# Kernel optimization log

Measured on AMD Instinct MI355X. Metric: run time of the kernel, lower is better.

## Reference

```python
import jax, jax.numpy as jnp
import numpy as np

B, S, D, E, H, K = 4, 2048, 1024, 8, 512, 2


def setup_inputs() -> dict:
    key = jax.random.key(0)
    ks = jax.random.split(key, 11)
    sc = 0.02
    return {
        "x": jax.random.normal(ks[0], (B, S, D), dtype=jnp.float32),
        "gate_W": jax.random.normal(ks[1], (D, E), dtype=jnp.float32) * sc,
        "W1": jax.random.normal(ks[2], (E, D, H), dtype=jnp.float32) * sc,
        "b1": jnp.zeros((E, H), dtype=jnp.float32),
        "W2": jax.random.normal(ks[3], (E, H, D), dtype=jnp.float32) * sc,
        "b2": jnp.zeros((E, D), dtype=jnp.float32),
        "Ws1": jax.random.normal(ks[4], (D, H), dtype=jnp.float32) * sc,
        "bs1": jnp.zeros((H,), dtype=jnp.float32),
        "Ws2": jax.random.normal(ks[5], (H, D), dtype=jnp.float32) * sc,
        "bs2": jnp.zeros((D,), dtype=jnp.float32),
        "route_scale": jnp.ones((), dtype=jnp.float32),
    }


def reference(x, gate_W, W1, b1, W2, b2, Ws1, bs1, Ws2, bs2, route_scale):
    # Gating: sigmoid scores scaled by route_scale (score_func='sigmoid')
    scores = jax.nn.sigmoid(x @ gate_W) * route_scale          # (B,S,E)
    topk_scores, topk_idx = jax.lax.top_k(scores, K)           # (B,S,K)
    topk_w = topk_scores / topk_scores.sum(-1, keepdims=True)  # normalized weights
    # Dense combine weights: zero for non-selected experts (same math as
    # the original sparse gather/scatter loop).
    onehot = jax.nn.one_hot(topk_idx, E, dtype=x.dtype)        # (B,S,K,E)
    gate_full = jnp.einsum('bsk,bske->bse', topk_w, onehot)    # (B,S,E)
    # Per-expert MLP applied to all tokens, combined with sparse gate weights.
    h = jax.nn.gelu(jnp.einsum('bsd,edh->bseh', x, W1) + b1, approximate=False)
    y = jnp.einsum('bseh,ehd->bsed', h, W2) + b2               # (B,S,E,D)
    expert_out = jnp.einsum('bse,bsed->bsd', gate_full, y)     # (B,S,D)
    # Shared expert MLP (always active)
    shared = jax.nn.gelu(x @ Ws1 + bs1, approximate=False) @ Ws2 + bs2
    return expert_out + shared
```

## Files before the change

kernel.cpp:

```cpp
#include <hip/hip_runtime.h>
#include <hip/hip_bf16.h>

#define TOKENS 8192
#define D_DIM  1024
#define E_NUM  8
#define H_DIM  512
#define N1     4608
#define CAP    3072
#define ET256  (CAP / 256)
#define EXP_ROWS (E_NUM * CAP)
#define SH_BASE  EXP_ROWS
#define HS_ROWS (EXP_ROWS + TOKENS)

typedef __bf16 bf16_t;
typedef __bf16 bf16x8 __attribute__((ext_vector_type(8)));
typedef __bf16 bf16x4 __attribute__((ext_vector_type(4)));
typedef float  f32x4  __attribute__((ext_vector_type(4)));

__device__ __forceinline__ float gelu_fast(float v) {
  float w = v * v;
  float t = __builtin_fmaf(w, 0.10294307f, 2.30258835f);
  float z = v * t;
  float e = __builtin_amdgcn_exp2f(z);
  float r = __builtin_amdgcn_rcpf(e + 1.0f);
  return v - v * r;
}

__global__ __launch_bounds__(256) void routing_repack_kernel(
    const float* __restrict__ x, const float* __restrict__ gW,
    const float* __restrict__ route_scale, float* __restrict__ gateT,
    int* __restrict__ sel, bf16_t* __restrict__ Xb,
    const float* __restrict__ W1, const float* __restrict__ Ws1,
    const float* __restrict__ W2, const float* __restrict__ Ws2,
    bf16_t* __restrict__ Bt1, bf16_t* __restrict__ Bt2e) {
  const int bid = blockIdx.x;
  if (bid < TOKENS / 4) {
    int tok  = bid * 4 + (threadIdx.x >> 6);
    int lane = threadIdx.x & 63;
    const float* xr = x + (size_t)tok * D_DIM;
    double p[E_NUM];
#pragma unroll
    for (int e = 0; e < E_NUM; ++e) p[e] = 0.0;
    for (int d = lane; d < D_DIM; d += 64) {
      double xv = (double)xr[d];
      const float* g = gW + (size_t)d * E_NUM;
#pragma unroll
      for (int e = 0; e < E_NUM; ++e) p[e] += xv * (double)g[e];
    }
#pragma unroll
    for (int off = 32; off > 0; off >>= 1) {
#pragma unroll
      for (int e = 0; e < E_NUM; ++e) p[e] += __shfl_xor(p[e], off, 64);
    }
    if (lane == 0) {
      double rs = (double)route_scale[0];
      double s[E_NUM];
#pragma unroll
      for (int e = 0; e < E_NUM; ++e) s[e] = rs / (1.0 + exp(-p[e]));
      int i1 = 0;
#pragma unroll
      for (int e = 1; e < E_NUM; ++e) if (s[e] > s[i1]) i1 = e;
      int i2 = (i1 == 0) ? 1 : 0;
#pragma unroll
      for (int e = 0; e < E_NUM; ++e) if (e != i1 && s[e] > s[i2]) i2 = e;
      double inv = 1.0 / (s[i1] + s[i2]);
      float o[E_NUM];
#pragma unroll
      for (int e = 0; e < E_NUM; ++e) o[e] = 0.f;
      o[i1] = (float)(s[i1] * inv);
      o[i2] = (float)(s[i2] * inv);
#pragma unroll
      for (int e = 0; e < E_NUM; ++e) gateT[(size_t)e * TOKENS + tok] = o[e];
      sel[tok] = i1 * 8 + i2;
    }
    const float4* x4 = (const float4*)xr;
    bf16x4* xb4 = (bf16x4*)(Xb + (size_t)tok * D_DIM);
#pragma unroll
    for (int i = 0; i < 4; ++i) {
      float4 v = x4[i * 64 + lane];
      bf16x4 o = { (bf16_t)v.x, (bf16_t)v.y, (bf16_t)v.z, (bf16_t)v.w };
      xb4[i * 64 + lane] = o;
    }
  } else {
    __shared__ float tile[32][33];
    const int rid = bid - TOKENS / 4;
    const int bx = rid & 31, by = rid >> 5;
    const int tx = threadIdx.x & 31, ty = threadIdx.x >> 5;
    if (by < 144) {
      const int k0 = bx * 32, n0 = by * 32;
#pragma unroll
      for (int i = 0; i < 4; ++i) {
        int kl = ty + i * 8;
        int n = n0 + tx, k = k0 + kl;
        float v;
        if (n0 < 4096) v = W1[(size_t)(n >> 9) * (D_DIM * H_DIM) + (size_t)k * H_DIM + (n & 511)];
        else           v = Ws1[(size_t)k * H_DIM + (n - 4096)];
        tile[kl][tx] = v;
      }
      __syncthreads();
#pragma unroll
      for (int i = 0; i < 4; ++i) {
        int nl = ty + i * 8;
        Bt1[(size_t)(n0 + nl) * D_DIM + k0 + tx] = (bf16_t)tile[tx][nl];
      }
    } else {
      const int yy = by - 144;
      const int e = yy >> 4;
      const int h0 = (yy & 15) * 32;
      const int d0 = bx * 32;
#pragma unroll
      for (int i = 0; i < 4; ++i) {
        int hl = ty + i * 8;
        int h = h0 + hl, d = d0 + tx;
        float v = (e < E_NUM) ? W2[((size_t)e * H_DIM + h) * D_DIM + d]
                              : Ws2[(size_t)h * D_DIM + d];
        tile[hl][tx] = v;
      }
      __syncthreads();
#pragma unroll
      for (int i = 0; i < 4; ++i) {
        int dl = ty + i * 8;
        Bt2e[((size_t)e * D_DIM + (d0 + dl)) * H_DIM + h0 + tx] = (bf16_t)tile[tx][dl];
      }
    }
  }
}

__global__ __launch_bounds__(256) void listbuild_kernel(
    const float* __restrict__ gateT, const int* __restrict__ sel,
    int* __restrict__ perm, float* __restrict__ grow,
    int* __restrict__ tok2row, int* __restrict__ padcnt) {
  const int e = blockIdx.x;
  const int tid = threadIdx.x, lane = tid & 63, wid = tid >> 6;
  __shared__ int wsum[4];
  const float* row = gateT + (size_t)e * TOKENS;
  const int base = e * CAP;
  int running = 0;
  float gv = row[tid];
  for (int c = 0; c < TOKENS / 256; ++c) {
    float gv_next = (c + 1 < TOKENS / 256) ? row[(c + 1) * 256 + tid] : 0.f;
    const int tok = c * 256 + tid;
    const bool f = gv > 0.f;
    unsigned long long m = __ballot(f);
    int lanepre = __popcll(m & ((1ull << lane) - 1ull));
    if (lane == 0) wsum[wid] = __popcll(m);
    __syncthreads();
    int wbase = 0;
#pragma unroll
    for (int w2 = 0; w2 < 4; ++w2) if (w2 < wid) wbase += wsum[w2];
    const int tot = wsum[0] + wsum[1] + wsum[2] + wsum[3];
    if (f) {
      const int idx = running + wbase + lanepre;
      if (idx < CAP) {
        perm[base + idx] = tok;
        grow[base + idx] = gv;
        const int s = sel[tok];
        const int other = ((s >> 3) == e) ? (s & 7) : (s >> 3);
        tok2row[tok * 2 + (e > other ? 1 : 0)] = base + idx;
      }
    }
    running += tot;
    __syncthreads();
    gv = gv_next;
  }
  if (running > CAP) running = CAP;
  const int pc = (running + 255) & ~255;
  for (int i = running + tid; i < pc; i += 256) { perm[base + i] = 0; grow[base + i] = 0.f; }
  if (tid == 0) padcnt[e] = pc;
}

__device__ __forceinline__ void gload16(const char* src, char* dst) {
  __builtin_amdgcn_global_load_lds((const __attribute__((address_space(1))) void*)src,
      (__attribute__((address_space(3))) void*)dst, 16, 0, 0);
}

__device__ __forceinline__ void gemm_core256(
    const char* ga0, const char* ga1, const char* ga2, const char* ga3,
    const char* gb0, const char* gb1, const char* gb2, const char* gb3,
    int ktiles, char* lds, int wid, int lane, f32x4 (&acc)[8][4]) {
  const int wm = wid >> 2, wn = wid & 3;
  const int lA = lane & 15, kq = lane >> 4;
  const int slot0 = (kq ^ (lA & 7)) * 16;
  const int slot1 = ((4 + kq) ^ (lA & 7)) * 16;

  auto stage8 = [&](int buf, int t) {
    char* dA = lds + buf * 65536 + wid * 1024;
    char* dB = dA + 32768;
    const size_t ko = (size_t)t * 128;
    gload16(ga0 + ko, dA + 0 * 8192);
    gload16(ga1 + ko, dA + 1 * 8192);
    gload16(ga2 + ko, dA + 2 * 8192);
    gload16(ga3 + ko, dA + 3 * 8192);
    gload16(gb0 + ko, dB + 0 * 8192);
    gload16(gb1 + ko, dB + 1 * 8192);
    gload16(gb2 + ko, dB + 2 * 8192);
    gload16(gb3 + ko, dB + 3 * 8192);
  };

  stage8(0, 0);
  for (int t = 0; t < ktiles; ++t) {
    const int b = t & 1;
    asm volatile("s_waitcnt vmcnt(0)" ::: "memory");
    __builtin_amdgcn_s_barrier();
    asm volatile("" ::: "memory");
    if (t + 1 < ktiles) stage8(b ^ 1, t + 1);
    const char* Ab = lds + b * 65536 + wm * 16384;
    const char* Bb = lds + b * 65536 + 32768 + (wn >> 1) * 16384 + ((wn & 1) * 64) * 128;
    bf16x8 bfv[4][2], af[8][2];
#pragma unroll
    for (int nf = 0; nf < 4; ++nf) {
      const int rb = (nf * 16 + lA) * 128;
      bfv[nf][0] = *(const bf16x8*)(Bb + rb + slot0);
      bfv[nf][1] = *(const bf16x8*)(Bb + rb + slot1);
    }
#pragma unroll
    for (int i = 0; i < 8; ++i) {
      const int ra = (i * 16 + lA) * 128;
      af[i][0] = *(const bf16x8*)(Ab + ra + slot0);
      af[i][1] = *(const bf16x8*)(Ab + ra + slot1);
    }
    __builtin_amdgcn_s_setprio(1);
#pragma unroll
    for (int s = 0; s < 2; ++s)
#pragma unroll
      for (int i = 0; i < 8; ++i)
#pragma unroll
        for (int nf = 0; nf < 4; ++nf)
          acc[i][nf] = __builtin_amdgcn_mfma_f32_16x16x32_bf16(
              af[i][s], bfv[nf][s], acc[i][nf], 0, 0, 0);
    __builtin_amdgcn_s_setprio(0);
  }
}

__device__ __forceinline__ int swz_src(int lane) {
  return ((lane & 7) ^ ((lane >> 3) & 7)) * 16;
}

__global__ __launch_bounds__(512, 2) void gemm1e_kernel(
    const bf16_t* __restrict__ Xb, const bf16_t* __restrict__ Bt1,
    const int* __restrict__ perm, const float* __restrict__ grow,
    const int* __restrict__ padcnt,
    const float* __restrict__ b1, const float* __restrict__ bs1,
    bf16_t* __restrict__ Hs) {
  __shared__ bf16_t sL[65536];
  const int t = threadIdx.x, wid = t >> 6, lane = t & 63;
  const int L = blockIdx.x + 2 * blockIdx.y;
  const int xc = L & 7, ii = L >> 3;
  const int bx = xc >> 2;
  const int by = (xc & 3) * 32 + ii;
  int e, rowbase;
  if (by < E_NUM * ET256) {
    e = by / ET256;
    const int lt = by - e * ET256;
    if (lt * 256 >= padcnt[e]) return;
    rowbase = e * CAP + lt * 256;
  } else {
    e = E_NUM;
    rowbase = SH_BASE + (by - E_NUM * ET256) * 256;
  }
  const int n0 = bx * 256;
  const int rl = wid * 8 + (lane >> 3);
  const int sc = swz_src(lane);
  const char *ga[4], *gb[4];
#pragma unroll
  for (int g = 0; g < 4; ++g) {
    const int r = g * 64 + rl;
    const int tok = (e < E_NUM) ? perm[rowbase + r] : (rowbase - SH_BASE + r);
    ga[g] = (const char*)Xb + (size_t)tok * 2048 + sc;
    gb[g] = (const char*)(Bt1 + (size_t)e * H_DIM * D_DIM) + (size_t)(n0 + r) * 2048 + sc;
  }
  f32x4 acc[8][4];
#pragma unroll
  for (int i = 0; i < 8; ++i)
#pragma unroll
    for (int j = 0; j < 4; ++j) acc[i][j] = (f32x4){0.f, 0.f, 0.f, 0.f};
  gemm_core256(ga[0], ga[1], ga[2], ga[3], gb[0], gb[1], gb[2], gb[3],
               D_DIM / 64, (char*)sL, wid, lane, acc);

  const int wm = wid >> 2, wn = wid & 3, lA = lane & 15;
  const float* bias = (e < E_NUM) ? (b1 + e * H_DIM) : bs1;
#pragma unroll
  for (int mf = 0; mf < 8; ++mf) {
    const int rloc = wm * 128 + mf * 16 + (lane >> 4) * 4;
    float gr[4];
#pragma unroll
    for (int q = 0; q < 4; ++q)
      gr[q] = (e < E_NUM) ? grow[rowbase + rloc + q] : 1.0f;
#pragma unroll
    for (int nf = 0; nf < 4; ++nf) {
      const int col = n0 + wn * 64 + nf * 16 + lA;
      const float bv = bias[col];
#pragma unroll
      for (int q = 0; q < 4; ++q) {
        float v = gelu_fast(acc[mf][nf][q] + bv);
        Hs[(size_t)(rowbase + rloc + q) * H_DIM + col] = (bf16_t)(v * gr[q]);
      }
    }
  }
}

__global__ __launch_bounds__(512, 2) void gemm2e_kernel(
    const bf16_t* __restrict__ Hs, const bf16_t* __restrict__ Bt2e,
    const float* __restrict__ grow, const int* __restrict__ padcnt,
    const float* __restrict__ b2, bf16_t* __restrict__ Ys) {
  __shared__ bf16_t sL[65536];
  const int t = threadIdx.x, wid = t >> 6, lane = t & 63;
  const int L = blockIdx.x + 4 * blockIdx.y;
  const int xc = L & 7, ii = L >> 3;
  const int bx = xc >> 1;
  const int by = (xc & 1) * 48 + ii;
  const int e = by / ET256;
  const int lt = by - e * ET256;
  if (lt * 256 >= padcnt[e]) return;
  const int rowbase = e * CAP + lt * 256;
  const int n0 = bx * 256;
  const int rl = wid * 8 + (lane >> 3);
  const int sc = swz_src(lane);
  const char *ga[4], *gb[4];
#pragma unroll
  for (int g = 0; g < 4; ++g) {
    const int r = g * 64 + rl;
    ga[g] = (const char*)Hs + (size_t)(rowbase + r) * 1024 + sc;
    gb[g] = (const char*)(Bt2e + (size_t)e * D_DIM * H_DIM) + (size_t)(n0 + r) * 1024 + sc;
  }
  f32x4 acc[8][4];
#pragma unroll
  for (int i = 0; i < 8; ++i)
#pragma unroll
    for (int j = 0; j < 4; ++j) acc[i][j] = (f32x4){0.f, 0.f, 0.f, 0.f};
  gemm_core256(ga[0], ga[1], ga[2], ga[3], gb[0], gb[1], gb[2], gb[3],
               H_DIM / 64, (char*)sL, wid, lane, acc);

  const int wm = wid >> 2, wn = wid & 3, lA = lane & 15;
  const float* bb = b2 + (size_t)e * D_DIM;
#pragma unroll
  for (int mf = 0; mf < 8; ++mf) {
    const int rloc = wm * 128 + mf * 16 + (lane >> 4) * 4;
    float gr[4];
#pragma unroll
    for (int q = 0; q < 4; ++q) gr[q] = grow[rowbase + rloc + q];
#pragma unroll
    for (int nf = 0; nf < 4; ++nf) {
      const int col = n0 + wn * 64 + nf * 16 + lA;
      const float bv = bb[col];
#pragma unroll
      for (int q = 0; q < 4; ++q)
        Ys[(size_t)(rowbase + rloc + q) * D_DIM + col] = (bf16_t)(acc[mf][nf][q] + gr[q] * bv);
    }
  }
}

__global__ __launch_bounds__(512, 2) void gemm2s_kernel(
    const bf16_t* __restrict__ Hs, const bf16_t* __restrict__ Bt2e,
    const int* __restrict__ tok2row, const float* __restrict__ bs2,
    const bf16_t* __restrict__ Ys, float* __restrict__ out) {
  __shared__ bf16_t sL[65536];
  const int t = threadIdx.x, wid = t >> 6, lane = t & 63;
  const int L = blockIdx.x + 4 * blockIdx.y;
  const int xc = L & 7, ii = L >> 3;
  const int bx = xc >> 1;
  const int by = (xc & 1) * 16 + ii;
  const int tokbase = by * 256;
  const int rowbase = SH_BASE + tokbase;
  const int n0 = bx * 256;
  const int rl = wid * 8 + (lane >> 3);
  const int sc = swz_src(lane);
  const char *ga[4], *gb[4];
#pragma unroll
  for (int g = 0; g < 4; ++g) {
    const int r = g * 64 + rl;
    ga[g] = (const char*)Hs + (size_t)(rowbase + r) * 1024 + sc;
    gb[g] = (const char*)(Bt2e + (size_t)E_NUM * D_DIM * H_DIM) + (size_t)(n0 + r) * 1024 + sc;
  }
  f32x4 acc[8][4];
#pragma unroll
  for (int i = 0; i < 8; ++i)
#pragma unroll
    for (int j = 0; j < 4; ++j) acc[i][j] = (f32x4){0.f, 0.f, 0.f, 0.f};
  gemm_core256(ga[0], ga[1], ga[2], ga[3], gb[0], gb[1], gb[2], gb[3],
               H_DIM / 64, (char*)sL, wid, lane, acc);

  const int wm = wid >> 2, wn = wid & 3, lA = lane & 15;
#pragma unroll
  for (int mf = 0; mf < 8; ++mf) {
    const int rloc = wm * 128 + mf * 16 + (lane >> 4) * 4;
    int r0[4], r1[4];
#pragma unroll
    for (int q = 0; q < 4; ++q) {
      const int tok = tokbase + rloc + q;
      r0[q] = tok2row[tok * 2];
      r1[q] = tok2row[tok * 2 + 1];
    }
#pragma unroll
    for (int nf = 0; nf < 4; ++nf) {
      const int col = n0 + wn * 64 + nf * 16 + lA;
      const float bv = bs2[col];
#pragma unroll
      for (int q = 0; q < 4; ++q) {
        const int tok = tokbase + rloc + q;
        float y0 = (float)Ys[(size_t)r0[q] * D_DIM + col];
        float y1 = (float)Ys[(size_t)r1[q] * D_DIM + col];
        out[(size_t)tok * D_DIM + col] = acc[mf][nf][q] + bv + y0 + y1;
      }
    }
  }
}

extern "C" void kernel_launch(void* const* d_in, const int* in_sizes, int n_in,
                              void* d_out, int out_size, void* d_ws, size_t ws_size,
                              hipStream_t stream) {
  (void)in_sizes; (void)n_in; (void)out_size; (void)ws_size;
  const float* x    = (const float*)d_in[0];
  const float* gW   = (const float*)d_in[1];
  const float* W1   = (const float*)d_in[2];
  const float* b1   = (const float*)d_in[3];
  const float* W2   = (const float*)d_in[4];
  const float* b2   = (const float*)d_in[5];
  const float* Ws1  = (const float*)d_in[6];
  const float* bs1  = (const float*)d_in[7];
  const float* Ws2  = (const float*)d_in[8];
  const float* bs2  = (const float*)d_in[9];
  const float* rsc  = (const float*)d_in[10];
  float* out = (float*)d_out;

  char* w = (char*)d_ws;
  float*  gateT = (float*)w;  w += (size_t)E_NUM * TOKENS * 4;
  int*    sel   = (int*)w;    w += (size_t)TOKENS * 4;
  bf16_t* Xb    = (bf16_t*)w; w += (size_t)TOKENS * D_DIM * 2;
  bf16_t* Bt1   = (bf16_t*)w; w += (size_t)N1 * D_DIM * 2;
  bf16_t* Bt2e  = (bf16_t*)w; w += (size_t)9 * D_DIM * H_DIM * 2;
  bf16_t* Hs    = (bf16_t*)w; w += (size_t)HS_ROWS * H_DIM * 2;
  bf16_t* Ys    = (bf16_t*)w; w += (size_t)EXP_ROWS * D_DIM * 2;
  int*    perm  = (int*)w;    w += (size_t)EXP_ROWS * 4;
  float*  grow  = (float*)w;  w += (size_t)EXP_ROWS * 4;
  int*    tok2row = (int*)w;  w += (size_t)TOKENS * 2 * 4;
  int*    padcnt  = (int*)w;

  routing_repack_kernel<<<TOKENS / 4 + 32 * 288, 256, 0, stream>>>(
      x, gW, rsc, gateT, sel, Xb, W1, Ws1, W2, Ws2, Bt1, Bt2e);
  listbuild_kernel<<<E_NUM, 256, 0, stream>>>(gateT, sel, perm, grow, tok2row, padcnt);

  gemm1e_kernel<<<dim3(H_DIM / 256, E_NUM * ET256 + TOKENS / 256), dim3(512), 0, stream>>>(
      Xb, Bt1, perm, grow, padcnt, b1, bs1, Hs);
  gemm2e_kernel<<<dim3(D_DIM / 256, E_NUM * ET256), dim3(512), 0, stream>>>(
      Hs, Bt2e, grow, padcnt, b2, Ys);
  gemm2s_kernel<<<dim3(D_DIM / 256, TOKENS / 256), dim3(512), 0, stream>>>(
      Hs, Bt2e, tok2row, bs2, Ys, out);
}
```

Before: 168.4 us.

## Shrink shared-expert GEMM2 tile to 128 rows and split A-fragment loads

```diff
diff --git a/kernel.cpp b/kernel.cpp
--- a/kernel.cpp
+++ b/kernel.cpp
@@ -206,7 +206,7 @@
     if (t + 1 < ktiles) stage8(b ^ 1, t + 1);
     const char* Ab = lds + b * 65536 + wm * 16384;
     const char* Bb = lds + b * 65536 + 32768 + (wn >> 1) * 16384 + ((wn & 1) * 64) * 128;
-    bf16x8 bfv[4][2], af[8][2];
+    bf16x8 bfv[4][2];
 #pragma unroll
     for (int nf = 0; nf < 4; ++nf) {
       const int rb = (nf * 16 + lA) * 128;
@@ -214,21 +214,87 @@
       bfv[nf][1] = *(const bf16x8*)(Bb + rb + slot1);
     }
 #pragma unroll
-    for (int i = 0; i < 8; ++i) {
-      const int ra = (i * 16 + lA) * 128;
-      af[i][0] = *(const bf16x8*)(Ab + ra + slot0);
-      af[i][1] = *(const bf16x8*)(Ab + ra + slot1);
-    }
-    __builtin_amdgcn_s_setprio(1);
-#pragma unroll
-    for (int s = 0; s < 2; ++s)
-#pragma unroll
-      for (int i = 0; i < 8; ++i)
-#pragma unroll
-        for (int nf = 0; nf < 4; ++nf)
-          acc[i][nf] = __builtin_amdgcn_mfma_f32_16x16x32_bf16(
-              af[i][s], bfv[nf][s], acc[i][nf], 0, 0, 0);
-    __builtin_amdgcn_s_setprio(0);
+    for (int qm = 0; qm < 2; ++qm) {
+      bf16x8 af[4][2];
+#pragma unroll
+      for (int i = 0; i < 4; ++i) {
+        const int ra = ((qm * 4 + i) * 16 + lA) * 128;
+        af[i][0] = *(const bf16x8*)(Ab + ra + slot0);
+        af[i][1] = *(const bf16x8*)(Ab + ra + slot1);
+      }
+      __builtin_amdgcn_s_setprio(1);
+#pragma unroll
+      for (int s = 0; s < 2; ++s)
+#pragma unroll
+        for (int i = 0; i < 4; ++i)
+#pragma unroll
+          for (int nf = 0; nf < 4; ++nf)
+            acc[qm * 4 + i][nf] = __builtin_amdgcn_mfma_f32_16x16x32_bf16(
+                af[i][s], bfv[nf][s], acc[qm * 4 + i][nf], 0, 0, 0);
+      __builtin_amdgcn_s_setprio(0);
+      __builtin_amdgcn_sched_barrier(0);
+    }
+  }
+}
+
+__device__ __forceinline__ void gemm_core_s(
+    const char* ga, const char* gb,
+    int ktiles, char* lds, int wid, int lane, f32x4 (&acc)[4][4]) {
+  const int wm = wid >> 2, wn = wid & 3;
+  const int lA = lane & 15, kq = lane >> 4;
+  const int slot0 = (kq ^ (lA & 7)) * 16;
+  const int slot1 = ((4 + kq) ^ (lA & 7)) * 16;
+
+  auto stage6 = [&](int buf, int t) {
+    char* base = lds + buf * 49152;
+    char* dA = base + wid * 2048;
+    char* dB = base + 16384 + wid * 4096;
+    const size_t ko = (size_t)t * 128;
+    gload16(ga + ko,         dA);
+    gload16(ga + 8192 + ko,  dA + 1024);
+    gload16(gb + ko,         dB);
+    gload16(gb + 8192 + ko,  dB + 1024);
+    gload16(gb + 16384 + ko, dB + 2048);
+    gload16(gb + 24576 + ko, dB + 3072);
+  };
+
+  stage6(0, 0);
+  for (int t = 0; t < ktiles; ++t) {
+    const int b = t & 1;
+    asm volatile("s_waitcnt vmcnt(0)" ::: "memory");
+    __builtin_amdgcn_s_barrier();
+    asm volatile("" ::: "memory");
+    if (t + 1 < ktiles) stage6(b ^ 1, t + 1);
+    const char* Ab = lds + b * 49152 + wm * 8192;
+    const char* Bb = lds + b * 49152 + 16384 + wn * 8192;
+    bf16x8 bfv[4][2];
+#pragma unroll
+    for (int nf = 0; nf < 4; ++nf) {
+      const int rb = (nf * 16 + lA) * 128;
+      bfv[nf][0] = *(const bf16x8*)(Bb + rb + slot0);
+      bfv[nf][1] = *(const bf16x8*)(Bb + rb + slot1);
+    }
+#pragma unroll
+    for (int qm = 0; qm < 2; ++qm) {
+      bf16x8 af[2][2];
+#pragma unroll
+      for (int i = 0; i < 2; ++i) {
+        const int ra = ((qm * 2 + i) * 16 + lA) * 128;
+        af[i][0] = *(const bf16x8*)(Ab + ra + slot0);
+        af[i][1] = *(const bf16x8*)(Ab + ra + slot1);
+      }
+      __builtin_amdgcn_s_setprio(1);
+#pragma unroll
+      for (int s = 0; s < 2; ++s)
+#pragma unroll
+        for (int i = 0; i < 2; ++i)
+#pragma unroll
+          for (int nf = 0; nf < 4; ++nf)
+            acc[qm * 2 + i][nf] = __builtin_amdgcn_mfma_f32_16x16x32_bf16(
+                af[i][s], bfv[nf][s], acc[qm * 2 + i][nf], 0, 0, 0);
+      __builtin_amdgcn_s_setprio(0);
+      __builtin_amdgcn_sched_barrier(0);
+    }
   }
 }
 
@@ -354,36 +420,30 @@
     const bf16_t* __restrict__ Hs, const bf16_t* __restrict__ Bt2e,
     const int* __restrict__ tok2row, const float* __restrict__ bs2,
     const bf16_t* __restrict__ Ys, float* __restrict__ out) {
-  __shared__ bf16_t sL[65536];
+  __shared__ bf16_t sL[49152];
   const int t = threadIdx.x, wid = t >> 6, lane = t & 63;
   const int L = blockIdx.x + 4 * blockIdx.y;
   const int xc = L & 7, ii = L >> 3;
   const int bx = xc >> 1;
-  const int by = (xc & 1) * 16 + ii;
-  const int tokbase = by * 256;
+  const int by = (xc & 1) * 32 + ii;
+  const int tokbase = by * 128;
   const int rowbase = SH_BASE + tokbase;
   const int n0 = bx * 256;
-  const int rl = wid * 8 + (lane >> 3);
   const int sc = swz_src(lane);
-  const char *ga[4], *gb[4];
-#pragma unroll
-  for (int g = 0; g < 4; ++g) {
-    const int r = g * 64 + rl;
-    ga[g] = (const char*)Hs + (size_t)(rowbase + r) * 1024 + sc;
-    gb[g] = (const char*)(Bt2e + (size_t)E_NUM * D_DIM * H_DIM) + (size_t)(n0 + r) * 1024 + sc;
-  }
-  f32x4 acc[8][4];
-#pragma unroll
-  for (int i = 0; i < 8; ++i)
+  const char* ga = (const char*)Hs + (size_t)(rowbase + wid * 16 + (lane >> 3)) * 1024 + sc;
+  const char* gb = (const char*)(Bt2e + (size_t)E_NUM * D_DIM * H_DIM)
+                 + (size_t)(n0 + wid * 32 + (lane >> 3)) * 1024 + sc;
+  f32x4 acc[4][4];
+#pragma unroll
+  for (int i = 0; i < 4; ++i)
 #pragma unroll
     for (int j = 0; j < 4; ++j) acc[i][j] = (f32x4){0.f, 0.f, 0.f, 0.f};
-  gemm_core256(ga[0], ga[1], ga[2], ga[3], gb[0], gb[1], gb[2], gb[3],
-               H_DIM / 64, (char*)sL, wid, lane, acc);
+  gemm_core_s(ga, gb, H_DIM / 64, (char*)sL, wid, lane, acc);
 
   const int wm = wid >> 2, wn = wid & 3, lA = lane & 15;
 #pragma unroll
-  for (int mf = 0; mf < 8; ++mf) {
-    const int rloc = wm * 128 + mf * 16 + (lane >> 4) * 4;
+  for (int mf = 0; mf < 4; ++mf) {
+    const int rloc = wm * 64 + mf * 16 + (lane >> 4) * 4;
     int r0[4], r1[4];
 #pragma unroll
     for (int q = 0; q < 4; ++q) {
@@ -444,6 +504,6 @@
       Xb, Bt1, perm, grow, padcnt, b1, bs1, Hs);
   gemm2e_kernel<<<dim3(D_DIM / 256, E_NUM * ET256), dim3(512), 0, stream>>>(
       Hs, Bt2e, grow, padcnt, b2, Ys);
-  gemm2s_kernel<<<dim3(D_DIM / 256, TOKENS / 256), dim3(512), 0, stream>>>(
+  gemm2s_kernel<<<dim3(D_DIM / 256, TOKENS / 128), dim3(512), 0, stream>>>(
       Hs, Bt2e, tok2row, bs2, Ys, out);
 }
```

After: 146.1 us. 13.3% less time.
